# Optimization experiments

Measured on AMD Instinct MI355X. Metric: run time of the kernel, lower is better.

Reference implementation:

```python
import jax, jax.numpy as jnp
import numpy as np

EPS = 1e-06

def setup_inputs() -> dict:
    key = jax.random.key(0)
    k1, k2, k3, k4, k5 = jax.random.split(key, 5)
    B, T, D, Dv = 4, 2048, 128, 128
    q = jax.random.normal(k1, (B, T, D), dtype=jnp.float32)
    k = jax.random.normal(k2, (B, T, D), dtype=jnp.float32)
    v = jax.random.normal(k3, (B, T, Dv), dtype=jnp.float32)
    # phi = nn.Linear(dim, dim) followed by ELU; torch Linear default init ~ U(-1/sqrt(D), 1/sqrt(D))
    lim = 1.0 / np.sqrt(D)
    W_phi = jax.random.uniform(k4, (D, D), minval=-lim, maxval=lim, dtype=jnp.float32)
    b_phi = jax.random.uniform(k5, (D,), minval=-lim, maxval=lim, dtype=jnp.float32)
    return {"q": q, "k": k, "v": v, "W_phi": W_phi, "b_phi": b_phi}

def reference(q, k, v, W_phi, b_phi):
    # feature map: phi(x) = ELU(x @ W^T + b) + 1  (positive features)
    def phi(x):
        return jax.nn.elu(jnp.einsum('btd,ed->bte', x, W_phi) + b_phi) + 1.0

    Q = phi(q)                      # [B,T,D]
    K = phi(k)                      # [B,T,D]
    # causal recurrent state (zero initial state since h=None):
    # z_t = sum_{tau<=t} K_tau                 -> [B,T,D]
    # s_t = sum_{tau<=t} K_tau (outer) v_tau   -> [B,T,D,Dv]
    z = jnp.cumsum(K, axis=1)
    s = jnp.cumsum(K[..., :, None] * v[..., None, :], axis=1)
    den = jnp.einsum('btd,btd->bt', Q, z) + EPS          # [B,T]
    out = jnp.einsum('btd,btde->bte', Q, s) / den[..., None]  # [B,T,Dv]
    return out
```

## Files before the change

kernel.cpp:

```cpp
#include <hip/hip_runtime.h>
#include <hip/hip_bf16.h>

#define BB 4
#define TT 2048
#define DD 128
#define CHK 64
#define NCHK 32
#define NCHKS (BB*NCHK)

typedef __attribute__((ext_vector_type(8))) short  bf16x8;
typedef __attribute__((ext_vector_type(4))) float  f32x4;

#define MFMA(a,b,c) __builtin_amdgcn_mfma_f32_16x16x32_bf16(a, b, c, 0, 0, 0)

__device__ __forceinline__ short f2b(float f) {
    union { float f; unsigned u; } x; x.f = f;
    unsigned r = x.u + 0x7fffu + ((x.u >> 16) & 1u);
    return (short)(r >> 16);
}
__device__ __forceinline__ float b2f(short s) {
    union { unsigned u; float f; } x; x.u = ((unsigned)(unsigned short)s) << 16;
    return x.f;
}
__device__ __forceinline__ bf16x8 cvt8(const float* p) {
    float4 a = *(const float4*)p, b = *(const float4*)(p + 4);
    bf16x8 r;
    r[0]=f2b(a.x); r[1]=f2b(a.y); r[2]=f2b(a.z); r[3]=f2b(a.w);
    r[4]=f2b(b.x); r[5]=f2b(b.y); r[6]=f2b(b.z); r[7]=f2b(b.w);
    return r;
}

__global__ __launch_bounds__(256) void k1_chunk(const float* __restrict__ q,
                                                const float* __restrict__ kin,
                                                const float* __restrict__ vin,
                                                const float* __restrict__ W,
                                                const float* __restrict__ bias,
                                                short* __restrict__ Ss_g,
                                                float* __restrict__ zc_g,
                                                short* __restrict__ vT_g,
                                                short* __restrict__ Qf_g,
                                                short* __restrict__ Kf_g) {
    int c = blockIdx.x >> 1, h = blockIdx.x & 1;
    const float* qc = q   + (size_t)c * CHK * DD;
    const float* kc = kin + (size_t)c * CHK * DD;
    const float* vc = vin + (size_t)c * CHK * DD;

    __shared__ __align__(16) short Wl  [DD][DD + 8];
    __shared__ __align__(16) short KfT [DD][CHK + 8];
    __shared__ __align__(16) short vT  [CHK][CHK + 8];
    __shared__ __align__(16) short stage[CHK][DD + 8];

    int tid = threadIdx.x, lane = tid & 63, w = tid >> 6;
    int l15 = lane & 15, l4 = lane >> 4;
    const f32x4 z4 = {0.f, 0.f, 0.f, 0.f};

    bf16x8 afk[4], afq[4];
    {
        int row = 16 * w + l15;
        #pragma unroll
        for (int kk = 0; kk < 4; ++kk) afk[kk] = cvt8(kc + row * DD + kk * 32 + l4 * 8);
        if (h) {
            #pragma unroll
            for (int kk = 0; kk < 4; ++kk) afq[kk] = cvt8(qc + row * DD + kk * 32 + l4 * 8);
        }
    }
    #pragma unroll
    for (int it = 0; it < 16; ++it) {
        int i = tid + it * 256;
        int row = i >> 5, c4 = (i & 31) * 4;
        float4 v = *(const float4*)(W + (size_t)row * DD + c4);
        unsigned lo = (unsigned short)f2b(v.x) | ((unsigned)(unsigned short)f2b(v.y) << 16);
        unsigned hi = (unsigned short)f2b(v.z) | ((unsigned)(unsigned short)f2b(v.w) << 16);
        uint2 p; p.x = lo; p.y = hi;
        *(uint2*)&Wl[row][c4] = p;
    }
    #pragma unroll
    for (int it = 0; it < 4; ++it) {
        int i = tid + it * 256;
        int t = i >> 4, c4 = (i & 15) * 4;
        float4 vv = *(const float4*)(vc + t * DD + 64 * h + c4);
        vT[c4 + 0][t] = f2b(vv.x); vT[c4 + 1][t] = f2b(vv.y);
        vT[c4 + 2][t] = f2b(vv.z); vT[c4 + 3][t] = f2b(vv.w);
    }
    __syncthreads();

    #pragma unroll
    for (int n = 0; n < 8; ++n) {
        int e = 16 * n + l15;
        f32x4 d = z4;
        #pragma unroll
        for (int kk = 0; kk < 4; ++kk) {
            bf16x8 bw = *(const bf16x8*)&Wl[e][kk * 32 + l4 * 8];
            d = MFMA(afk[kk], bw, d);
        }
        float bv = bias[e];
        #pragma unroll
        for (int j = 0; j < 4; ++j) {
            float zv = d[j] + bv;
            short r = f2b((zv > 0.f) ? (zv + 1.f) : __expf(zv));
            int t = 16 * w + l4 * 4 + j;
            KfT[e][t] = r;
            if (h == 0) stage[t][e] = r;
        }
    }
    if (h) {
        #pragma unroll
        for (int n = 0; n < 8; ++n) {
            int e = 16 * n + l15;
            f32x4 d = z4;
            #pragma unroll
            for (int kk = 0; kk < 4; ++kk) {
                bf16x8 bw = *(const bf16x8*)&Wl[e][kk * 32 + l4 * 8];
                d = MFMA(afq[kk], bw, d);
            }
            float bv = bias[e];
            #pragma unroll
            for (int j = 0; j < 4; ++j) {
                float zv = d[j] + bv;
                stage[16 * w + l4 * 4 + j][e] = f2b((zv > 0.f) ? (zv + 1.f) : __expf(zv));
            }
        }
    }
    __syncthreads();

    {
        short* dst = (h ? Qf_g : Kf_g) + (size_t)c * CHK * DD;
        #pragma unroll
        for (int it = 0; it < 4; ++it) {
            int i = tid + it * 256;
            int t = i >> 4, u = (i & 15) * 8;
            *(bf16x8*)(dst + t * DD + u) = *(const bf16x8*)&stage[t][u];
        }
    }
    if (h == 0 && tid < DD) {
        float s = 0.f;
        #pragma unroll
        for (int t8 = 0; t8 < CHK / 8; ++t8) {
            bf16x8 kv = *(const bf16x8*)&KfT[tid][t8 * 8];
            #pragma unroll
            for (int j = 0; j < 8; ++j) s += b2f(kv[j]);
        }
        zc_g[(size_t)c * DD + tid] = s;
    }
    #pragma unroll
    for (int it = 0; it < 2; ++it) {
        int i = tid + it * 256;
        int e = i >> 3, t0 = (i & 7) * 8;
        *(bf16x8*)(vT_g + (size_t)c * DD * CHK + (64 * h + e) * CHK + t0) =
            *(const bf16x8*)&vT[e][t0];
    }

    f32x4 sacc[2][4];
    #pragma unroll
    for (int mi = 0; mi < 2; ++mi)
        #pragma unroll
        for (int n = 0; n < 4; ++n) sacc[mi][n] = z4;
    #pragma unroll
    for (int kk = 0; kk < 2; ++kk) {
        bf16x8 afr[2];
        #pragma unroll
        for (int mi = 0; mi < 2; ++mi)
            afr[mi] = *(const bf16x8*)&KfT[16 * (2 * w + mi) + l15][kk * 32 + l4 * 8];
        #pragma unroll
        for (int n = 0; n < 4; ++n) {
            bf16x8 bfr = *(const bf16x8*)&vT[16 * n + l15][kk * 32 + l4 * 8];
            sacc[0][n] = MFMA(afr[0], bfr, sacc[0][n]);
            sacc[1][n] = MFMA(afr[1], bfr, sacc[1][n]);
        }
    }
    __syncthreads();

    #pragma unroll
    for (int mi = 0; mi < 2; ++mi)
        #pragma unroll
        for (int n = 0; n < 4; ++n) {
            int e = 16 * n + l15;
            #pragma unroll
            for (int j = 0; j < 4; ++j)
                stage[e][16 * (2 * w + mi) + l4 * 4 + j] = f2b(sacc[mi][n][j]);
        }
    __syncthreads();

    {
        short* dst = Ss_g + (size_t)c * DD * DD + (size_t)(64 * h) * DD;
        #pragma unroll
        for (int it = 0; it < 4; ++it) {
            int i = tid + it * 256;
            int e = i >> 4, u = (i & 15) * 8;
            *(bf16x8*)(dst + e * DD + u) = *(const bf16x8*)&stage[e][u];
        }
    }
}

__global__ __launch_bounds__(128) void k2_scan(const short* __restrict__ Ss_g,
                                               const float* __restrict__ zc_g,
                                               short* __restrict__ Sp_g,
                                               float* __restrict__ zp_g) {
    int e = blockIdx.x & 127, b = blockIdx.x >> 7;
    int d = threadIdx.x;
    size_t base = ((size_t)(b * NCHK) * DD + e) * DD + d;
    const size_t stride = (size_t)DD * DD;

    float vals[NCHK];
    #pragma unroll
    for (int c2 = 0; c2 < NCHK; ++c2) vals[c2] = b2f(Ss_g[base + c2 * stride]);
    float run = 0.f;
    #pragma unroll
    for (int c2 = 0; c2 < NCHK; ++c2) {
        Sp_g[base + c2 * stride] = f2b(run);
        run += vals[c2];
    }
    if (e == 0) {
        float vz[NCHK];
        #pragma unroll
        for (int c2 = 0; c2 < NCHK; ++c2) vz[c2] = zc_g[(size_t)(b * NCHK + c2) * DD + d];
        float rz = 0.f;
        #pragma unroll
        for (int c2 = 0; c2 < NCHK; ++c2) {
            zp_g[(size_t)(b * NCHK + c2) * DD + d] = rz;
            rz += vz[c2];
        }
    }
}

__global__ __launch_bounds__(256) void k3_out(const short* __restrict__ Qf_g,
                                              const short* __restrict__ Kf_g,
                                              const short* __restrict__ Sp_g,
                                              const float* __restrict__ zp_g,
                                              const short* __restrict__ vT_g,
                                              float* __restrict__ out) {
    int c = blockIdx.x >> 2, h2 = blockIdx.x & 3;

    __shared__ __align__(16) short Ps[CHK][CHK + 8];
    __shared__ float den[CHK];

    int tid = threadIdx.x, lane = tid & 63, w = tid >> 6;
    int l15 = lane & 15, l4 = lane >> 4;
    const f32x4 z4 = {0.f, 0.f, 0.f, 0.f};

    const short* Qc = Qf_g + (size_t)c * CHK * DD;
    const short* Kc = Kf_g + (size_t)c * CHK * DD;
    const float* zp = zp_g + (size_t)c * DD;

    bf16x8 aq[4];
    #pragma unroll
    for (int kk = 0; kk < 4; ++kk)
        aq[kk] = *(const bf16x8*)(Qc + (16 * w + l15) * DD + kk * 32 + l4 * 8);

    bf16x8 bz[4];
    #pragma unroll
    for (int kk = 0; kk < 4; ++kk) {
        bf16x8 zf = cvt8(zp + kk * 32 + l4 * 8);
        bf16x8 zero = {0,0,0,0,0,0,0,0};
        bz[kk] = (l15 == 0) ? zf : zero;
    }

    float rs[4] = {0.f, 0.f, 0.f, 0.f};
    f32x4 p4 = z4;
    #pragma unroll
    for (int kk = 0; kk < 4; ++kk) p4 = MFMA(aq[kk], bz[kk], p4);
    #pragma unroll
    for (int n2 = 0; n2 < 4; ++n2) {
        f32x4 p = z4;
        #pragma unroll
        for (int kk = 0; kk < 4; ++kk) {
            bf16x8 bk = *(const bf16x8*)(Kc + (16 * n2 + l15) * DD + kk * 32 + l4 * 8);
            p = MFMA(aq[kk], bk, p);
        }
        int t2 = 16 * n2 + l15;
        #pragma unroll
        for (int j = 0; j < 4; ++j) {
            int t = 16 * w + l4 * 4 + j;
            float pm = (t2 <= t) ? p[j] : 0.f;
            Ps[t][t2] = f2b(pm);
            rs[j] += pm;
        }
    }
    #pragma unroll
    for (int off = 1; off < 16; off <<= 1) {
        #pragma unroll
        for (int j = 0; j < 4; ++j) rs[j] += __shfl_xor(rs[j], off);
    }
    if (l15 == 0) {
        #pragma unroll
        for (int j = 0; j < 4; ++j)
            den[16 * w + l4 * 4 + j] = rs[j] + p4[j] + 1e-6f;
    }
    __syncthreads();

    bf16x8 ap[2];
    #pragma unroll
    for (int kk = 0; kk < 2; ++kk)
        ap[kk] = *(const bf16x8*)&Ps[16 * w + l15][kk * 32 + l4 * 8];

    const short* Sp  = Sp_g + (size_t)c * DD * DD;
    const short* vTg = vT_g + (size_t)c * DD * CHK;
    f32x4 oacc[2];
    oacc[0] = z4; oacc[1] = z4;
    #pragma unroll
    for (int n = 0; n < 2; ++n) {
        int e = 32 * h2 + 16 * n + l15;
        #pragma unroll
        for (int kk = 0; kk < 4; ++kk) {
            bf16x8 bs = *(const bf16x8*)(Sp + e * DD + kk * 32 + l4 * 8);
            oacc[n] = MFMA(aq[kk], bs, oacc[n]);
        }
        #pragma unroll
        for (int kk = 0; kk < 2; ++kk) {
            bf16x8 bv = *(const bf16x8*)(vTg + e * CHK + kk * 32 + l4 * 8);
            oacc[n] = MFMA(ap[kk], bv, oacc[n]);
        }
    }

    float* oc = out + (size_t)c * CHK * DD;
    float invs[4];
    #pragma unroll
    for (int j = 0; j < 4; ++j) invs[j] = 1.0f / den[16 * w + l4 * 4 + j];
    #pragma unroll
    for (int n = 0; n < 2; ++n) {
        int e = 32 * h2 + 16 * n + l15;
        #pragma unroll
        for (int j = 0; j < 4; ++j) {
            int t = 16 * w + l4 * 4 + j;
            oc[t * DD + e] = oacc[n][j] * invs[j];
        }
    }
}

extern "C" void kernel_launch(void* const* d_in, const int* in_sizes, int n_in,
                              void* d_out, int out_size, void* d_ws, size_t ws_size,
                              hipStream_t stream) {
    const float* q  = (const float*)d_in[0];
    const float* k  = (const float*)d_in[1];
    const float* v  = (const float*)d_in[2];
    const float* W  = (const float*)d_in[3];
    const float* bi = (const float*)d_in[4];
    float* out = (float*)d_out;

    float* zc_g = (float*)d_ws;
    float* zp_g = zc_g + (size_t)NCHKS * DD;
    short* Ss_g = (short*)(zp_g + (size_t)NCHKS * DD);
    short* Sp_g = Ss_g + (size_t)NCHKS * DD * DD;
    short* vT_g = Sp_g + (size_t)NCHKS * DD * DD;
    short* Qf_g = vT_g + (size_t)NCHKS * DD * CHK;
    short* Kf_g = Qf_g + (size_t)NCHKS * CHK * DD;

    k1_chunk<<<2 * NCHKS, 256, 0, stream>>>(q, k, v, W, bi, Ss_g, zc_g, vT_g, Qf_g, Kf_g);
    k2_scan<<<512, 128, 0, stream>>>(Ss_g, zc_g, Sp_g, zp_g);
    k3_out<<<4 * NCHKS, 256, 0, stream>>>(Qf_g, Kf_g, Sp_g, zp_g, vT_g, out);
}
```

Before: 32.10 us.

## Split chunk kernel by feature half and merge output blocks with LDS-staged Q/K

The chunk kernel no longer splits blocks into a K-half and a Q-half with unequal work. Each block now computes both the K and Q feature maps for 64 output features, using only half of W, plus a 64×128 slice of the chunk state, so work is balanced across blocks. The output kernel goes from four to two blocks per chunk. It stages Qf and Kf into LDS once so every wave reads from shared memory, and it drops one barrier. This trades fewer, heavier blocks and more LDS per block for less redundant global traffic and better load balance.

```diff
diff --git a/kernel.cpp b/kernel.cpp
--- a/kernel.cpp
+++ b/kernel.cpp
@@ -30,25 +30,26 @@
     return r;
 }
 
-__global__ __launch_bounds__(256) void k1_chunk(const float* __restrict__ q,
-                                                const float* __restrict__ kin,
-                                                const float* __restrict__ vin,
-                                                const float* __restrict__ W,
-                                                const float* __restrict__ bias,
-                                                short* __restrict__ Ss_g,
-                                                float* __restrict__ zc_g,
-                                                short* __restrict__ vT_g,
-                                                short* __restrict__ Qf_g,
-                                                short* __restrict__ Kf_g) {
-    int c = blockIdx.x >> 1, h = blockIdx.x & 1;
+__global__ __launch_bounds__(256, 2) void k1_chunk(const float* __restrict__ q,
+                                                   const float* __restrict__ kin,
+                                                   const float* __restrict__ vin,
+                                                   const float* __restrict__ W,
+                                                   const float* __restrict__ bias,
+                                                   short* __restrict__ Ss_g,
+                                                   float* __restrict__ zc_g,
+                                                   short* __restrict__ vT_g,
+                                                   short* __restrict__ Qf_g,
+                                                   short* __restrict__ Kf_g) {
+    int c = blockIdx.x >> 1, dh = blockIdx.x & 1;
+    int d0 = 64 * dh;
     const float* qc = q   + (size_t)c * CHK * DD;
     const float* kc = kin + (size_t)c * CHK * DD;
     const float* vc = vin + (size_t)c * CHK * DD;
 
-    __shared__ __align__(16) short Wl  [DD][DD + 8];
-    __shared__ __align__(16) short KfT [DD][CHK + 8];
-    __shared__ __align__(16) short vT  [CHK][CHK + 8];
-    __shared__ __align__(16) short stage[CHK][DD + 8];
+    __shared__ __align__(16) short Wl [64][DD + 8];
+    __shared__ __align__(16) short KfT[64][CHK + 8];
+    __shared__ __align__(16) short vT [DD][CHK + 8];
+    __shared__ __align__(16) short stage[2][CHK][CHK + 8];
 
     int tid = threadIdx.x, lane = tid & 63, w = tid >> 6;
     int l15 = lane & 15, l4 = lane >> 4;
@@ -58,81 +59,67 @@
     {
         int row = 16 * w + l15;
         #pragma unroll
-        for (int kk = 0; kk < 4; ++kk) afk[kk] = cvt8(kc + row * DD + kk * 32 + l4 * 8);
-        if (h) {
-            #pragma unroll
-            for (int kk = 0; kk < 4; ++kk) afq[kk] = cvt8(qc + row * DD + kk * 32 + l4 * 8);
-        }
-    }
-    #pragma unroll
-    for (int it = 0; it < 16; ++it) {
+        for (int kk = 0; kk < 4; ++kk) {
+            afk[kk] = cvt8(kc + row * DD + kk * 32 + l4 * 8);
+            afq[kk] = cvt8(qc + row * DD + kk * 32 + l4 * 8);
+        }
+    }
+    #pragma unroll
+    for (int it = 0; it < 8; ++it) {
         int i = tid + it * 256;
         int row = i >> 5, c4 = (i & 31) * 4;
-        float4 v = *(const float4*)(W + (size_t)row * DD + c4);
+        float4 v = *(const float4*)(W + (size_t)(d0 + row) * DD + c4);
         unsigned lo = (unsigned short)f2b(v.x) | ((unsigned)(unsigned short)f2b(v.y) << 16);
         unsigned hi = (unsigned short)f2b(v.z) | ((unsigned)(unsigned short)f2b(v.w) << 16);
         uint2 p; p.x = lo; p.y = hi;
         *(uint2*)&Wl[row][c4] = p;
     }
     #pragma unroll
-    for (int it = 0; it < 4; ++it) {
+    for (int it = 0; it < 8; ++it) {
         int i = tid + it * 256;
-        int t = i >> 4, c4 = (i & 15) * 4;
-        float4 vv = *(const float4*)(vc + t * DD + 64 * h + c4);
-        vT[c4 + 0][t] = f2b(vv.x); vT[c4 + 1][t] = f2b(vv.y);
-        vT[c4 + 2][t] = f2b(vv.z); vT[c4 + 3][t] = f2b(vv.w);
-    }
-    __syncthreads();
-
-    #pragma unroll
-    for (int n = 0; n < 8; ++n) {
-        int e = 16 * n + l15;
-        f32x4 d = z4;
+        int t = i >> 5, e4 = (i & 31) * 4;
+        float4 vv = *(const float4*)(vc + t * DD + e4);
+        vT[e4 + 0][t] = f2b(vv.x); vT[e4 + 1][t] = f2b(vv.y);
+        vT[e4 + 2][t] = f2b(vv.z); vT[e4 + 3][t] = f2b(vv.w);
+    }
+    __syncthreads();
+
+    #pragma unroll
+    for (int n = 0; n < 4; ++n) {
+        int dl = 16 * n + l15;
+        f32x4 dk = z4, dq = z4;
         #pragma unroll
         for (int kk = 0; kk < 4; ++kk) {
-            bf16x8 bw = *(const bf16x8*)&Wl[e][kk * 32 + l4 * 8];
-            d = MFMA(afk[kk], bw, d);
-        }
-        float bv = bias[e];
+            bf16x8 bw = *(const bf16x8*)&Wl[dl][kk * 32 + l4 * 8];
+            dk = MFMA(afk[kk], bw, dk);
+            dq = MFMA(afq[kk], bw, dq);
+        }
+        float bv = bias[d0 + dl];
         #pragma unroll
         for (int j = 0; j < 4; ++j) {
-            float zv = d[j] + bv;
-            short r = f2b((zv > 0.f) ? (zv + 1.f) : __expf(zv));
             int t = 16 * w + l4 * 4 + j;
-            KfT[e][t] = r;
-            if (h == 0) stage[t][e] = r;
-        }
-    }
-    if (h) {
-        #pragma unroll
-        for (int n = 0; n < 8; ++n) {
-            int e = 16 * n + l15;
-            f32x4 d = z4;
-            #pragma unroll
-            for (int kk = 0; kk < 4; ++kk) {
-                bf16x8 bw = *(const bf16x8*)&Wl[e][kk * 32 + l4 * 8];
-                d = MFMA(afq[kk], bw, d);
-            }
-            float bv = bias[e];
-            #pragma unroll
-            for (int j = 0; j < 4; ++j) {
-                float zv = d[j] + bv;
-                stage[16 * w + l4 * 4 + j][e] = f2b((zv > 0.f) ? (zv + 1.f) : __expf(zv));
-            }
+            float zk = dk[j] + bv;
+            short rk = f2b((zk > 0.f) ? (zk + 1.f) : __expf(zk));
+            KfT[dl][t] = rk;
+            stage[0][t][dl] = rk;
+            float zq = dq[j] + bv;
+            stage[1][t][dl] = f2b((zq > 0.f) ? (zq + 1.f) : __expf(zq));
         }
     }
     __syncthreads();
 
     {
-        short* dst = (h ? Qf_g : Kf_g) + (size_t)c * CHK * DD;
-        #pragma unroll
-        for (int it = 0; it < 4; ++it) {
+        short* dk_ = Kf_g + (size_t)c * CHK * DD + d0;
+        short* dq_ = Qf_g + (size_t)c * CHK * DD + d0;
+        #pragma unroll
+        for (int it = 0; it < 2; ++it) {
             int i = tid + it * 256;
-            int t = i >> 4, u = (i & 15) * 8;
-            *(bf16x8*)(dst + t * DD + u) = *(const bf16x8*)&stage[t][u];
-        }
-    }
-    if (h == 0 && tid < DD) {
+            int t = i >> 3, u = (i & 7) * 8;
+            *(bf16x8*)(dk_ + t * DD + u) = *(const bf16x8*)&stage[0][t][u];
+            *(bf16x8*)(dq_ + t * DD + u) = *(const bf16x8*)&stage[1][t][u];
+        }
+    }
+    if (tid < 64) {
         float s = 0.f;
         #pragma unroll
         for (int t8 = 0; t8 < CHK / 8; ++t8) {
@@ -140,55 +127,48 @@
             #pragma unroll
             for (int j = 0; j < 8; ++j) s += b2f(kv[j]);
         }
-        zc_g[(size_t)c * DD + tid] = s;
-    }
-    #pragma unroll
-    for (int it = 0; it < 2; ++it) {
-        int i = tid + it * 256;
-        int e = i >> 3, t0 = (i & 7) * 8;
-        *(bf16x8*)(vT_g + (size_t)c * DD * CHK + (64 * h + e) * CHK + t0) =
-            *(const bf16x8*)&vT[e][t0];
-    }
-
-    f32x4 sacc[2][4];
-    #pragma unroll
-    for (int mi = 0; mi < 2; ++mi)
-        #pragma unroll
-        for (int n = 0; n < 4; ++n) sacc[mi][n] = z4;
-    #pragma unroll
-    for (int kk = 0; kk < 2; ++kk) {
-        bf16x8 afr[2];
-        #pragma unroll
-        for (int mi = 0; mi < 2; ++mi)
-            afr[mi] = *(const bf16x8*)&KfT[16 * (2 * w + mi) + l15][kk * 32 + l4 * 8];
-        #pragma unroll
-        for (int n = 0; n < 4; ++n) {
-            bf16x8 bfr = *(const bf16x8*)&vT[16 * n + l15][kk * 32 + l4 * 8];
-            sacc[0][n] = MFMA(afr[0], bfr, sacc[0][n]);
-            sacc[1][n] = MFMA(afr[1], bfr, sacc[1][n]);
-        }
-    }
-    __syncthreads();
-
-    #pragma unroll
-    for (int mi = 0; mi < 2; ++mi)
-        #pragma unroll
-        for (int n = 0; n < 4; ++n) {
-            int e = 16 * n + l15;
-            #pragma unroll
-            for (int j = 0; j < 4; ++j)
-                stage[e][16 * (2 * w + mi) + l4 * 4 + j] = f2b(sacc[mi][n][j]);
-        }
-    __syncthreads();
-
-    {
-        short* dst = Ss_g + (size_t)c * DD * DD + (size_t)(64 * h) * DD;
+        zc_g[(size_t)c * DD + d0 + tid] = s;
+    }
+    if (dh == 0) {
         #pragma unroll
         for (int it = 0; it < 4; ++it) {
             int i = tid + it * 256;
-            int e = i >> 4, u = (i & 15) * 8;
-            *(bf16x8*)(dst + e * DD + u) = *(const bf16x8*)&stage[e][u];
-        }
+            int e = i >> 3, t0 = (i & 7) * 8;
+            *(bf16x8*)(vT_g + (size_t)c * DD * CHK + e * CHK + t0) =
+                *(const bf16x8*)&vT[e][t0];
+        }
+    }
+
+    f32x4 sacc[8];
+    #pragma unroll
+    for (int n = 0; n < 8; ++n) sacc[n] = z4;
+    #pragma unroll
+    for (int kk = 0; kk < 2; ++kk) {
+        bf16x8 afr = *(const bf16x8*)&KfT[16 * w + l15][kk * 32 + l4 * 8];
+        #pragma unroll
+        for (int n = 0; n < 8; ++n) {
+            bf16x8 bfr = *(const bf16x8*)&vT[16 * n + l15][kk * 32 + l4 * 8];
+            sacc[n] = MFMA(afr, bfr, sacc[n]);
+        }
+    }
+    __syncthreads();
+
+    short (*st)[CHK + 8] = (short(*)[CHK + 8])&stage[0][0][0];
+    #pragma unroll
+    for (int n = 0; n < 8; ++n) {
+        int e = 16 * n + l15;
+        #pragma unroll
+        for (int j = 0; j < 4; ++j)
+            st[e][16 * w + l4 * 4 + j] = f2b(sacc[n][j]);
+    }
+    __syncthreads();
+
+    short* dst = Ss_g + (size_t)c * DD * DD + d0;
+    #pragma unroll
+    for (int it = 0; it < 4; ++it) {
+        int i = tid + it * 256;
+        int e = i >> 3, u = (i & 7) * 8;
+        *(bf16x8*)(dst + e * DD + u) = *(const bf16x8*)&st[e][u];
     }
 }
 
@@ -229,8 +209,10 @@
                                               const float* __restrict__ zp_g,
                                               const short* __restrict__ vT_g,
                                               float* __restrict__ out) {
-    int c = blockIdx.x >> 2, h2 = blockIdx.x & 3;
-
+    int c = blockIdx.x >> 1, h = blockIdx.x & 1;
+
+    __shared__ __align__(16) short Qf[CHK][DD + 8];
+    __shared__ __align__(16) short Kf[CHK][DD + 8];
     __shared__ __align__(16) short Ps[CHK][CHK + 8];
     __shared__ float den[CHK];
 
@@ -238,15 +220,7 @@
     int l15 = lane & 15, l4 = lane >> 4;
     const f32x4 z4 = {0.f, 0.f, 0.f, 0.f};
 
-    const short* Qc = Qf_g + (size_t)c * CHK * DD;
-    const short* Kc = Kf_g + (size_t)c * CHK * DD;
     const float* zp = zp_g + (size_t)c * DD;
-
-    bf16x8 aq[4];
-    #pragma unroll
-    for (int kk = 0; kk < 4; ++kk)
-        aq[kk] = *(const bf16x8*)(Qc + (16 * w + l15) * DD + kk * 32 + l4 * 8);
-
     bf16x8 bz[4];
     #pragma unroll
     for (int kk = 0; kk < 4; ++kk) {
@@ -255,16 +229,35 @@
         bz[kk] = (l15 == 0) ? zf : zero;
     }
 
+    {
+        const short* srcq = Qf_g + (size_t)c * CHK * DD;
+        const short* srck = Kf_g + (size_t)c * CHK * DD;
+        #pragma unroll
+        for (int it = 0; it < 4; ++it) {
+            int i = tid + it * 256;
+            int t = i >> 4, u = (i & 15) * 8;
+            *(bf16x8*)&Qf[t][u] = *(const bf16x8*)(srcq + t * DD + u);
+            *(bf16x8*)&Kf[t][u] = *(const bf16x8*)(srck + t * DD + u);
+        }
+    }
+    __syncthreads();
+
+    bf16x8 aq[4];
+    #pragma unroll
+    for (int kk = 0; kk < 4; ++kk)
+        aq[kk] = *(const bf16x8*)&Qf[16 * w + l15][kk * 32 + l4 * 8];
+
+    f32x4 p4 = z4;
+    #pragma unroll
+    for (int kk = 0; kk < 4; ++kk) p4 = MFMA(aq[kk], bz[kk], p4);
+
     float rs[4] = {0.f, 0.f, 0.f, 0.f};
-    f32x4 p4 = z4;
-    #pragma unroll
-    for (int kk = 0; kk < 4; ++kk) p4 = MFMA(aq[kk], bz[kk], p4);
     #pragma unroll
     for (int n2 = 0; n2 < 4; ++n2) {
         f32x4 p = z4;
         #pragma unroll
         for (int kk = 0; kk < 4; ++kk) {
-            bf16x8 bk = *(const bf16x8*)(Kc + (16 * n2 + l15) * DD + kk * 32 + l4 * 8);
+            bf16x8 bk = *(const bf16x8*)&Kf[16 * n2 + l15][kk * 32 + l4 * 8];
             p = MFMA(aq[kk], bk, p);
         }
         int t2 = 16 * n2 + l15;
@@ -286,7 +279,6 @@
         for (int j = 0; j < 4; ++j)
             den[16 * w + l4 * 4 + j] = rs[j] + p4[j] + 1e-6f;
     }
-    __syncthreads();
 
     bf16x8 ap[2];
     #pragma unroll
@@ -295,11 +287,12 @@
 
     const short* Sp  = Sp_g + (size_t)c * DD * DD;
     const short* vTg = vT_g + (size_t)c * DD * CHK;
-    f32x4 oacc[2];
-    oacc[0] = z4; oacc[1] = z4;
-    #pragma unroll
-    for (int n = 0; n < 2; ++n) {
-        int e = 32 * h2 + 16 * n + l15;
+    f32x4 oacc[4];
+    #pragma unroll
+    for (int n = 0; n < 4; ++n) oacc[n] = z4;
+    #pragma unroll
+    for (int n = 0; n < 4; ++n) {
+        int e = 64 * h + 16 * n + l15;
         #pragma unroll
         for (int kk = 0; kk < 4; ++kk) {
             bf16x8 bs = *(const bf16x8*)(Sp + e * DD + kk * 32 + l4 * 8);
@@ -317,8 +310,8 @@
     #pragma unroll
     for (int j = 0; j < 4; ++j) invs[j] = 1.0f / den[16 * w + l4 * 4 + j];
     #pragma unroll
-    for (int n = 0; n < 2; ++n) {
-        int e = 32 * h2 + 16 * n + l15;
+    for (int n = 0; n < 4; ++n) {
+        int e = 64 * h + 16 * n + l15;
         #pragma unroll
         for (int j = 0; j < 4; ++j) {
             int t = 16 * w + l4 * 4 + j;
@@ -347,5 +340,5 @@
 
     k1_chunk<<<2 * NCHKS, 256, 0, stream>>>(q, k, v, W, bi, Ss_g, zc_g, vT_g, Qf_g, Kf_g);
     k2_scan<<<512, 128, 0, stream>>>(Ss_g, zc_g, Sp_g, zp_g);
-    k3_out<<<4 * NCHKS, 256, 0, stream>>>(Qf_g, Kf_g, Sp_g, zp_g, vT_g, out);
-}
+    k3_out<<<2 * NCHKS, 256, 0, stream>>>(Qf_g, Kf_g, Sp_g, zp_g, vT_g, out);
+}
```

Measured after the change: 27.02 us (median of 2 runs). 15.8% less time.
